# Performance work log

Hardware: AMD Instinct MI355X
Metric: run time of the kernel (lower is better)

Reference implementation:

```python
import jax, jax.numpy as jnp
import numpy as np

N, F, P, E, HID = 50000, 4, 12, 1_600_000, 64  # nodes, input feats, periods (FH), edges, hidden


def setup_inputs() -> dict:
    key = jax.random.key(0)
    ks = jax.random.split(key, 16)

    def nrm(k, shp, scale=0.1):
        return jax.random.normal(k, shp, jnp.float32) * scale

    inp = {
        "x": jax.random.normal(ks[0], (N, F, P), jnp.float32),
        "edge_index": jax.random.randint(ks[1], (2, E), 0, N),
        "edge_weights": jax.random.uniform(ks[2], (E,), jnp.float32),
        "att": nrm(ks[3], (P,), 1.0),
    }
    i = 4
    for g in ("z", "r", "h"):  # TGCN gate params: GCNConv weight/bias + Linear(2*hid, hid)
        inp[f"Wg_{g}"] = nrm(ks[i], (F, HID))
        inp[f"bg_{g}"] = jnp.zeros((HID,), jnp.float32)
        inp[f"Wl_{g}"] = nrm(jax.random.fold_in(ks[i], 1), (2 * HID, HID))
        inp[f"bl_{g}"] = jnp.zeros((HID,), jnp.float32)
        i += 1
    for j in range(1, 5):
        inp[f"W{j}"] = nrm(ks[i], (HID, HID))
        inp[f"b{j}"] = jnp.zeros((HID,), jnp.float32)
        i += 1
    inp["Wo"] = nrm(ks[i], (HID, P * F))
    inp["bo"] = jnp.zeros((P * F,), jnp.float32)
    return inp


def _gcn_norm(edge_index, ew):
    # GCNConv default: add self loops (weight 1), symmetric D^-1/2 (A+I) D^-1/2 normalization
    src, dst = edge_index[0], edge_index[1]
    loop = jnp.arange(N)
    src_f = jnp.concatenate([src, loop])
    dst_f = jnp.concatenate([dst, loop])
    ew_f = jnp.concatenate([ew, jnp.ones((N,), ew.dtype)])
    deg = jax.ops.segment_sum(ew_f, dst_f, num_segments=N)
    dinv = jnp.where(deg > 0, jax.lax.rsqrt(deg), 0.0)
    norm = dinv[src_f] * ew_f * dinv[dst_f]
    return src_f, dst_f, norm


def _gcn(x, W, b, src, dst, norm):
    xw = x @ W                               # [N, HID] transform before propagate
    msg = xw[src] * norm[:, None]            # gather + scale, [E+N, HID]
    return jax.ops.segment_sum(msg, dst, num_segments=N) + b


def reference(x, edge_index, edge_weights, att,
              Wg_z, bg_z, Wl_z, bl_z,
              Wg_r, bg_r, Wl_r, bl_r,
              Wg_h, bg_h, Wl_h, bl_h,
              W1, b1, W2, b2, W3, b3, W4, b4, Wo, bo):
    src, dst, norm = _gcn_norm(edge_index, edge_weights)

    def tgcn_cell(xt):
        # A3TGCN passes H=None every period -> H starts at zeros each period
        Hz = jnp.zeros((xt.shape[0], HID), xt.dtype)
        z = jax.nn.sigmoid(jnp.concatenate([_gcn(xt, Wg_z, bg_z, src, dst, norm), Hz], -1) @ Wl_z + bl_z)
        r = jax.nn.sigmoid(jnp.concatenate([_gcn(xt, Wg_r, bg_r, src, dst, norm), Hz], -1) @ Wl_r + bl_r)
        htil = jnp.tanh(jnp.concatenate([_gcn(xt, Wg_h, bg_h, src, dst, norm), Hz * r], -1) @ Wl_h + bl_h)
        return z * Hz + (1.0 - z) * htil

    probs = jax.nn.softmax(att)
    h = jnp.zeros((N, HID), x.dtype)
    for p in range(P):  # small fixed period loop keeps peak memory at one period's messages
        h = h + probs[p] * tgcn_cell(x[:, :, p])

    h = jax.nn.relu(h)
    h = h @ W1 + b1
    h = h @ W2 + b2
    h = h @ W3 + b3
    h = h @ W4 + b4
    h = h @ Wo + bo                          # [N, FH*F]
    return h.reshape(-1, F, P)
```

## Files before the change

kernel.cpp:

```cpp
#include <hip/hip_runtime.h>
#include <hip/hip_fp16.h>

#define FP 48
#define HID 64
#define NP 12
#define PL 65
#define NBB 256
#define BT 1024
#define CAPB 17920

__device__ __forceinline__ void mm_stage(const float* __restrict__ Alds,
                                         const float* __restrict__ Wg,
                                         float* __restrict__ Clds, int t)
{
    const int rg = (t >> 4) * 4, cg = (t & 15) * 4;
    float acc[4][4] = {};
    for (int k = 0; k < 64; ++k) {
        float a0 = Alds[(rg + 0) * PL + k];
        float a1 = Alds[(rg + 1) * PL + k];
        float a2 = Alds[(rg + 2) * PL + k];
        float a3 = Alds[(rg + 3) * PL + k];
        const float4 bv = *reinterpret_cast<const float4*>(Wg + k * 64 + cg);
        acc[0][0] += a0 * bv.x; acc[0][1] += a0 * bv.y; acc[0][2] += a0 * bv.z; acc[0][3] += a0 * bv.w;
        acc[1][0] += a1 * bv.x; acc[1][1] += a1 * bv.y; acc[1][2] += a1 * bv.z; acc[1][3] += a1 * bv.w;
        acc[2][0] += a2 * bv.x; acc[2][1] += a2 * bv.y; acc[2][2] += a2 * bv.z; acc[2][3] += a2 * bv.w;
        acc[3][0] += a3 * bv.x; acc[3][1] += a3 * bv.y; acc[3][2] += a3 * bv.z; acc[3][3] += a3 * bv.w;
    }
    for (int i = 0; i < 4; ++i)
        for (int j = 0; j < 4; ++j)
            Clds[(rg + i) * PL + cg + j] = acc[i][j];
}

__device__ __forceinline__ void bias_stage(const float* __restrict__ bin,
                                           const float* __restrict__ Wg,
                                           const float* __restrict__ badd,
                                           float* __restrict__ bout, int t)
{
    if (t < 64) {
        float s = badd[t];
        for (int k = 0; k < 64; ++k) s += bin[k] * Wg[k * 64 + t];
        bout[t] = s;
    }
}

__device__ void do_prep(
    const float* __restrict__ att,
    const float* __restrict__ Wg_z, const float* __restrict__ bg_z,
    const float* __restrict__ Wl_z, const float* __restrict__ bl_z,
    const float* __restrict__ Wg_h, const float* __restrict__ bg_h,
    const float* __restrict__ Wl_h, const float* __restrict__ bl_h,
    const float* __restrict__ W1, const float* __restrict__ b1,
    const float* __restrict__ W2, const float* __restrict__ b2,
    const float* __restrict__ W3, const float* __restrict__ b3,
    const float* __restrict__ W4, const float* __restrict__ b4,
    const float* __restrict__ Wo, const float* __restrict__ bo,
    float* __restrict__ probs, float* __restrict__ Mz, float* __restrict__ cz,
    float* __restrict__ Mh, float* __restrict__ ch,
    float* __restrict__ Wc, float* __restrict__ bc, int t)
{
    __shared__ float A[64 * PL];
    __shared__ float B[64 * PL];
    __shared__ float bias[64];
    __shared__ float bias2[64];

    if (t == 0) {
        float m = att[0];
        for (int p = 1; p < NP; ++p) m = fmaxf(m, att[p]);
        float e[NP]; float s = 0.f;
        for (int p = 0; p < NP; ++p) { e[p] = __expf(att[p] - m); s += e[p]; }
        float inv = 1.f / s;
        for (int p = 0; p < NP; ++p) probs[p] = e[p] * inv;
    }

    if (t < 256) {
        int f = t >> 6, j = t & 63;
        float az = 0.f, ah = 0.f;
        for (int k = 0; k < HID; ++k) {
            az += Wg_z[f * HID + k] * Wl_z[k * HID + j];
            ah += Wg_h[f * HID + k] * Wl_h[k * HID + j];
        }
        Mz[t] = az; Mh[t] = ah;
    }
    if (t < HID) {
        float az = bl_z[t], ah = bl_h[t];
        for (int k = 0; k < HID; ++k) {
            az += bg_z[k] * Wl_z[k * HID + t];
            ah += bg_h[k] * Wl_h[k * HID + t];
        }
        cz[t] = az; ch[t] = ah;
    }

    for (int idx = t; idx < 4096; idx += BT) {
        int i = idx >> 6, j = idx & 63;
        A[i * PL + j] = W1[idx];
    }
    if (t < 64) bias[t] = b1[t];
    __syncthreads();

    if (t < 256) mm_stage(A, W2, B, t);
    bias_stage(bias, W2, b2, bias2, t);
    __syncthreads();
    if (t < 256) mm_stage(B, W3, A, t);
    bias_stage(bias2, W3, b3, bias, t);
    __syncthreads();
    if (t < 256) mm_stage(A, W4, B, t);
    bias_stage(bias, W4, b4, bias2, t);
    __syncthreads();

    if (t < 256) {
        const int rg = (t >> 4) * 4, cg = (t & 15) * 4;
        if (cg < FP) {
            float acc[4][4] = {};
            for (int k = 0; k < 64; ++k) {
                float a0 = B[(rg + 0) * PL + k];
                float a1 = B[(rg + 1) * PL + k];
                float a2 = B[(rg + 2) * PL + k];
                float a3 = B[(rg + 3) * PL + k];
                const float4 bv = *reinterpret_cast<const float4*>(Wo + k * FP + cg);
                acc[0][0] += a0 * bv.x; acc[0][1] += a0 * bv.y; acc[0][2] += a0 * bv.z; acc[0][3] += a0 * bv.w;
                acc[1][0] += a1 * bv.x; acc[1][1] += a1 * bv.y; acc[1][2] += a1 * bv.z; acc[1][3] += a1 * bv.w;
                acc[2][0] += a2 * bv.x; acc[2][1] += a2 * bv.y; acc[2][2] += a2 * bv.z; acc[2][3] += a2 * bv.w;
                acc[3][0] += a3 * bv.x; acc[3][1] += a3 * bv.y; acc[3][2] += a3 * bv.z; acc[3][3] += a3 * bv.w;
            }
            for (int i = 0; i < 4; ++i)
                for (int j = 0; j < 4; ++j)
                    Wc[(rg + i) * FP + cg + j] = acc[i][j];
        }
        if (t < FP) {
            float s = bo[t];
            for (int k = 0; k < 64; ++k) s += bias2[k] * Wo[k * FP + t];
            bc[t] = s;
        }
    }
}

__global__ __launch_bounds__(BT) void build_kernel(
    const int* __restrict__ src, const int* __restrict__ dst,
    const float* __restrict__ ew,
    unsigned* __restrict__ cursor, int2* __restrict__ binned,
    int E, int CE, int NBUK,
    const float* __restrict__ att,
    const float* __restrict__ Wg_z, const float* __restrict__ bg_z,
    const float* __restrict__ Wl_z, const float* __restrict__ bl_z,
    const float* __restrict__ Wg_h, const float* __restrict__ bg_h,
    const float* __restrict__ Wl_h, const float* __restrict__ bl_h,
    const float* __restrict__ W1, const float* __restrict__ b1,
    const float* __restrict__ W2, const float* __restrict__ b2,
    const float* __restrict__ W3, const float* __restrict__ b3,
    const float* __restrict__ W4, const float* __restrict__ b4,
    const float* __restrict__ Wo, const float* __restrict__ bo,
    float* __restrict__ probs, float* __restrict__ Mz, float* __restrict__ cz,
    float* __restrict__ Mh, float* __restrict__ ch,
    float* __restrict__ Wc, float* __restrict__ bc)
{
    const int t = threadIdx.x;
    if (blockIdx.x == NBB) {
        do_prep(att, Wg_z, bg_z, Wl_z, bl_z, Wg_h, bg_h, Wl_h, bl_h,
                W1, b1, W2, b2, W3, b3, W4, b4, Wo, bo,
                probs, Mz, cz, Mh, ch, Wc, bc, t);
        return;
    }
    __shared__ int cnt[128];
    __shared__ int off[128];
    const int base = blockIdx.x * CE;
    const int endb = min(base + CE, E);
    if (t < NBUK) cnt[t] = 0;
    __syncthreads();
    for (int e = base + t; e < endb; e += BT)
        atomicAdd(&cnt[((unsigned)dst[e]) >> 9], 1);
    __syncthreads();
    if (t < NBUK) {
        const int c = cnt[t];
        off[t] = c ? (int)atomicAdd(&cursor[t], (unsigned)c) : 0;
    }
    __syncthreads();
    for (int e = base + t; e < endb; e += BT) {
        const int d = dst[e];
        const int b = ((unsigned)d) >> 9;
        const int r = atomicAdd(&off[b], 1);
        if (r < CAPB)
            binned[(size_t)b * CAPB + r] =
                make_int2(((d & 511) << 16) | src[e], __float_as_int(ew[e]));
    }
}

__global__ __launch_bounds__(1024) void csr_convert_kernel(
    const int2* __restrict__ binned, const unsigned* __restrict__ cursor,
    unsigned* __restrict__ csr, int2* __restrict__ nodeinfo,
    const float* __restrict__ x,
    unsigned short* __restrict__ xs, int N, int NBUK)
{
    const int t = threadIdx.x;
    const int b = blockIdx.x;
    const int node0 = b << 9;
    const int nend = min(512, N - node0);
    const int ebeg = b * CAPB;
    const int ecnt = min((int)cursor[b], CAPB);
    const int eend = ebeg + ecnt;

    __shared__ int   cnt[512];
    __shared__ float fsum[512];
    __shared__ int   pfx[512];
    __shared__ float sdi[512];

    if (t < 512) { cnt[t] = 0; fsum[t] = 0.f; }
    __syncthreads();

    for (int e = ebeg + t; e < eend; e += 1024) {
        const int2 v = binned[e];
        const int dl = (v.x >> 16) & 511;
        atomicAdd(&cnt[dl], 1);
        atomicAdd(&fsum[dl], __int_as_float(v.y));
    }
    __syncthreads();

    const int myc = (t < 512) ? cnt[t] : 0;
    if (t < 512) pfx[t] = myc;
    __syncthreads();
    for (int off = 1; off < 512; off <<= 1) {
        int tmp = (t >= off && t < 512) ? pfx[t - off] : 0;
        __syncthreads();
        if (t < 512) pfx[t] += tmp;
        __syncthreads();
    }

    if (t < 512) {
        const int excl = pfx[t] - myc;
        const float di = rsqrtf(1.f + fsum[t]);
        sdi[t] = di;
        if (t < nend)
            nodeinfo[node0 + t] = make_int2((myc << 22) | (ebeg + excl), __float_as_int(di));
        cnt[t] = ebeg + excl;
    }
    __syncthreads();

    for (int e = ebeg + t; e < eend; e += 1024) {
        const int2 v = binned[e];
        const int dl = (v.x >> 16) & 511;
        const int pos = atomicAdd(&cnt[dl], 1);
        const float w = __int_as_float(v.y);
        const unsigned hb = (unsigned)__half_as_ushort(__float2half_rn(w));
        csr[pos] = (unsigned)(v.x & 0xffff) | (hb << 16);
    }

    const int gtot = nend * 6;
    for (int g = t; g < gtot; g += 1024) {
        const int nl = g / 6;
        const int q = g - nl * 6;
        const float dsc = sdi[nl];
        const float* xr = x + (size_t)(node0 + nl) * FP + q * 8;
        const float4 v0 = *reinterpret_cast<const float4*>(xr);
        const float4 v1 = *reinterpret_cast<const float4*>(xr + 4);
        unsigned p0 = (unsigned)__half_as_ushort(__float2half_rn(dsc * v0.x)) |
                      ((unsigned)__half_as_ushort(__float2half_rn(dsc * v0.y)) << 16);
        unsigned p1 = (unsigned)__half_as_ushort(__float2half_rn(dsc * v0.z)) |
                      ((unsigned)__half_as_ushort(__float2half_rn(dsc * v0.w)) << 16);
        unsigned p2 = (unsigned)__half_as_ushort(__float2half_rn(dsc * v1.x)) |
                      ((unsigned)__half_as_ushort(__float2half_rn(dsc * v1.y)) << 16);
        unsigned p3 = (unsigned)__half_as_ushort(__float2half_rn(dsc * v1.z)) |
                      ((unsigned)__half_as_ushort(__float2half_rn(dsc * v1.w)) << 16);
        *reinterpret_cast<int4*>(xs + (size_t)(node0 + nl) * FP + q * 8) =
            make_int4((int)p0, (int)p1, (int)p2, (int)p3);
    }
}

__global__ __launch_bounds__(256) void gather_node_kernel(
    const unsigned short* __restrict__ xs, const float* __restrict__ x,
    const int2* __restrict__ nodeinfo,
    const unsigned* __restrict__ csr,
    const float* __restrict__ probs,
    const float* __restrict__ Mz, const float* __restrict__ cz,
    const float* __restrict__ Mh, const float* __restrict__ ch,
    const float* __restrict__ Wc, const float* __restrict__ bc,
    float* __restrict__ out, int N)
{
    __shared__ __align__(16) float sWc[HID * FP];
    __shared__ __align__(16) float sprobs[16];
    __shared__ __align__(16) float yacc[4][384];
    __shared__ __align__(16) float yld[4][FP];
    __shared__ __align__(16) float hld[4][HID];
    for (int i = threadIdx.x; i < HID * FP; i += 256) sWc[i] = Wc[i];
    if (threadIdx.x < NP) sprobs[threadIdx.x] = probs[threadIdx.x];
    __syncthreads();

    const int lane = threadIdx.x & 63;
    const int wib  = threadIdx.x >> 6;
    const int n    = blockIdx.x * 4 + wib;
    if (n >= N) return;

    const int slot = lane >> 3;
    const int q    = lane & 7;
    const bool act = (q < 6);
    const int qc   = act ? q : 5;
    const char* xsb = (const char*)xs;

    const int2 ni = nodeinfo[n];
    const int beg = ni.x & 0x3FFFFF;
    const int end = beg + (int)((unsigned)ni.x >> 22);
    const float di = __int_as_float(ni.y);

    float a0 = 0.f, a1 = 0.f, a2 = 0.f, a3 = 0.f;
    float a4 = 0.f, a5 = 0.f, a6 = 0.f, a7 = 0.f;
    #pragma unroll 2
    for (int e = beg + slot; e < end; e += 8) {
        const unsigned ev = csr[e];
        const float w = __half2float(__ushort_as_half((unsigned short)(ev >> 16)));
        const unsigned soff = (ev & 0xffffu) * 96u;
        const int4 xv = *reinterpret_cast<const int4*>(xsb + soff + (qc << 4));
        const float2 f0 = __half22float2(*reinterpret_cast<const __half2*>(&xv.x));
        const float2 f1 = __half22float2(*reinterpret_cast<const __half2*>(&xv.y));
        const float2 f2 = __half22float2(*reinterpret_cast<const __half2*>(&xv.z));
        const float2 f3 = __half22float2(*reinterpret_cast<const __half2*>(&xv.w));
        a0 = fmaf(w, f0.x, a0); a1 = fmaf(w, f0.y, a1);
        a2 = fmaf(w, f1.x, a2); a3 = fmaf(w, f1.y, a3);
        a4 = fmaf(w, f2.x, a4); a5 = fmaf(w, f2.y, a5);
        a6 = fmaf(w, f3.x, a6); a7 = fmaf(w, f3.y, a7);
    }

    if (act) {
        float* dst0 = &yacc[wib][slot * 48 + q * 8];
        *reinterpret_cast<float4*>(dst0)     = make_float4(a0, a1, a2, a3);
        *reinterpret_cast<float4*>(dst0 + 4) = make_float4(a4, a5, a6, a7);
    }

    if (lane < FP) {
        const float* yf = yacc[wib];
        float s = 0.f;
        #pragma unroll
        for (int sl = 0; sl < 8; ++sl) s += yf[sl * 48 + lane];
        float xself = x[(size_t)n * FP + lane];
        float yv = di * s + di * di * xself;
        int f = lane / 12;
        int p = lane - f * 12;
        yld[wib][p * 4 + f] = yv;
    }

    const float mz0 = Mz[lane], mz1 = Mz[64 + lane], mz2 = Mz[128 + lane], mz3 = Mz[192 + lane];
    const float mh0 = Mh[lane], mh1 = Mh[64 + lane], mh2 = Mh[128 + lane], mh3 = Mh[192 + lane];
    const float czv = cz[lane], chv = ch[lane];
    const int   c   = (lane < FP) ? lane : 0;
    const float bcv = bc[c];

    const float* yw = yld[wib];
    float hacc = 0.f;
    #pragma unroll
    for (int p = 0; p < NP; ++p) {
        const float4 v = *reinterpret_cast<const float4*>(yw + p * 4);
        float az = czv + v.x * mz0 + v.y * mz1 + v.z * mz2 + v.w * mz3;
        float ah = chv + v.x * mh0 + v.y * mh1 + v.z * mh2 + v.w * mh3;
        float g  = __builtin_amdgcn_rcpf(1.f + __expf(az));
        float ahc = fminf(fmaxf(ah, -15.f), 15.f);
        float eh = __expf(2.f * ahc);
        float th = 1.f - 2.f * __builtin_amdgcn_rcpf(eh + 1.f);
        hacc += sprobs[p] * g * th;
    }
    hacc = fmaxf(hacc, 0.f);

    hld[wib][lane] = hacc;
    const float* hw = hld[wib];
    float o = bcv;
    #pragma unroll
    for (int i4 = 0; i4 < 16; ++i4) {
        const float4 h4 = *reinterpret_cast<const float4*>(hw + i4 * 4);
        o += h4.x * sWc[(i4 * 4 + 0) * FP + c];
        o += h4.y * sWc[(i4 * 4 + 1) * FP + c];
        o += h4.z * sWc[(i4 * 4 + 2) * FP + c];
        o += h4.w * sWc[(i4 * 4 + 3) * FP + c];
    }
    if (lane < FP) out[(size_t)n * FP + lane] = o;
}

extern "C" void kernel_launch(void* const* d_in, const int* in_sizes, int n_in,
                              void* d_out, int out_size, void* d_ws, size_t ws_size,
                              hipStream_t stream)
{
    const int N = in_sizes[0] / FP;
    const int E = in_sizes[1] / 2;
    const int NBUK = (N + 511) >> 9;
    const int CE = (E + NBB - 1) / NBB;

    const float* x    = (const float*)d_in[0];
    const int*   ei   = (const int*)d_in[1];
    const float* ew   = (const float*)d_in[2];
    const float* att  = (const float*)d_in[3];
    const float* Wg_z = (const float*)d_in[4];
    const float* bg_z = (const float*)d_in[5];
    const float* Wl_z = (const float*)d_in[6];
    const float* bl_z = (const float*)d_in[7];
    const float* Wg_h = (const float*)d_in[12];
    const float* bg_h = (const float*)d_in[13];
    const float* Wl_h = (const float*)d_in[14];
    const float* bl_h = (const float*)d_in[15];
    const float* W1 = (const float*)d_in[16]; const float* b1 = (const float*)d_in[17];
    const float* W2 = (const float*)d_in[18]; const float* b2 = (const float*)d_in[19];
    const float* W3 = (const float*)d_in[20]; const float* b3 = (const float*)d_in[21];
    const float* W4 = (const float*)d_in[22]; const float* b4 = (const float*)d_in[23];
    const float* Wo = (const float*)d_in[24]; const float* bo = (const float*)d_in[25];

    const int* srcp = ei;
    const int* dstp = ei + E;

    int2* binned       = (int2*)d_ws;
    unsigned* csr      = (unsigned*)(binned + (size_t)NBUK * CAPB);
    unsigned short* xs = (unsigned short*)(csr + (size_t)NBUK * CAPB);
    unsigned* cursor   = (unsigned*)(xs + (size_t)N * FP);
    int2* nodeinfo     = (int2*)(cursor + 128);
    float* probs       = (float*)(nodeinfo + N);
    float* Mz          = probs + 16;
    float* cz          = Mz + 256;
    float* Mh          = cz + 64;
    float* ch          = Mh + 256;
    float* Wc          = ch + 64;
    float* bc          = Wc + HID * FP;

    hipMemsetAsync(cursor, 0, (size_t)NBUK * sizeof(unsigned), stream);

    build_kernel<<<NBB + 1, BT, 0, stream>>>(
        srcp, dstp, ew, cursor, binned, E, CE, NBUK,
        att, Wg_z, bg_z, Wl_z, bl_z, Wg_h, bg_h, Wl_h, bl_h,
        W1, b1, W2, b2, W3, b3, W4, b4, Wo, bo,
        probs, Mz, cz, Mh, ch, Wc, bc);

    csr_convert_kernel<<<NBUK, 1024, 0, stream>>>(binned, cursor, csr, nodeinfo,
                                                  x, xs, N, NBUK);

    gather_node_kernel<<<(N + 3) / 4, 256, 0, stream>>>(xs, x, nodeinfo, csr,
                                                        probs, Mz, cz, Mh, ch, Wc, bc,
                                                        (float*)d_out, N);
}
```

Measured before the change: 273.3 us.

## Use finer 128-node buckets, more build blocks, register-cached CSR conversion

Shrinks the destination buckets from 512 to 128 nodes, giving about 391 buckets. This spreads the CSR conversion over many more, smaller 512-thread blocks instead of 98 blocks of 1024 threads. The build kernel now uses 512 edge blocks and staggers its cursor atomics by block index to reduce contention. The conversion kernel loads each bucket's edges into registers once and reuses them for counting and scattering, rather than reading global memory twice. The cost is a fixed per-bucket capacity of 4864, only 10 edges per thread, and silent edge drops if a bucket overflows.

```diff
diff --git a/kernel.cpp b/kernel.cpp
--- a/kernel.cpp
+++ b/kernel.cpp
@@ -5,9 +5,10 @@
 #define HID 64
 #define NP 12
 #define PL 65
-#define NBB 256
+#define NBB 512
 #define BT 1024
-#define CAPB 17920
+#define CAPB 4864
+#define NBKMAX 512
 
 __device__ __forceinline__ void mm_stage(const float* __restrict__ Alds,
                                          const float* __restrict__ Wg,
@@ -160,31 +161,32 @@
                 probs, Mz, cz, Mh, ch, Wc, bc, t);
         return;
     }
-    __shared__ int cnt[128];
-    __shared__ int off[128];
+    __shared__ int cnt[NBKMAX];
+    __shared__ int off[NBKMAX];
     const int base = blockIdx.x * CE;
     const int endb = min(base + CE, E);
-    if (t < NBUK) cnt[t] = 0;
+    for (int i = t; i < NBUK; i += BT) cnt[i] = 0;
     __syncthreads();
     for (int e = base + t; e < endb; e += BT)
-        atomicAdd(&cnt[((unsigned)dst[e]) >> 9], 1);
-    __syncthreads();
-    if (t < NBUK) {
-        const int c = cnt[t];
-        off[t] = c ? (int)atomicAdd(&cursor[t], (unsigned)c) : 0;
+        atomicAdd(&cnt[((unsigned)dst[e]) >> 7], 1);
+    __syncthreads();
+    for (int i = t; i < NBUK; i += BT) {
+        const int idx = (i + (int)blockIdx.x) % NBUK;
+        const int c = cnt[idx];
+        off[idx] = c ? (int)atomicAdd(&cursor[idx], (unsigned)c) : 0;
     }
     __syncthreads();
     for (int e = base + t; e < endb; e += BT) {
         const int d = dst[e];
-        const int b = ((unsigned)d) >> 9;
-        const int r = atomicAdd(&off[b], 1);
+        const int bk = ((unsigned)d) >> 7;
+        const int r = atomicAdd(&off[bk], 1);
         if (r < CAPB)
-            binned[(size_t)b * CAPB + r] =
-                make_int2(((d & 511) << 16) | src[e], __float_as_int(ew[e]));
-    }
-}
-
-__global__ __launch_bounds__(1024) void csr_convert_kernel(
+            binned[(size_t)bk * CAPB + r] =
+                make_int2(((d & 127) << 16) | src[e], __float_as_int(ew[e]));
+    }
+}
+
+__global__ __launch_bounds__(512) void csr_convert_kernel(
     const int2* __restrict__ binned, const unsigned* __restrict__ cursor,
     unsigned* __restrict__ csr, int2* __restrict__ nodeinfo,
     const float* __restrict__ x,
@@ -192,39 +194,47 @@
 {
     const int t = threadIdx.x;
     const int b = blockIdx.x;
-    const int node0 = b << 9;
-    const int nend = min(512, N - node0);
+    const int node0 = b << 7;
+    const int nend = min(128, N - node0);
     const int ebeg = b * CAPB;
     const int ecnt = min((int)cursor[b], CAPB);
-    const int eend = ebeg + ecnt;
-
-    __shared__ int   cnt[512];
-    __shared__ float fsum[512];
-    __shared__ int   pfx[512];
-    __shared__ float sdi[512];
-
-    if (t < 512) { cnt[t] = 0; fsum[t] = 0.f; }
-    __syncthreads();
-
-    for (int e = ebeg + t; e < eend; e += 1024) {
-        const int2 v = binned[e];
-        const int dl = (v.x >> 16) & 511;
-        atomicAdd(&cnt[dl], 1);
-        atomicAdd(&fsum[dl], __int_as_float(v.y));
-    }
-    __syncthreads();
-
-    const int myc = (t < 512) ? cnt[t] : 0;
-    if (t < 512) pfx[t] = myc;
-    __syncthreads();
-    for (int off = 1; off < 512; off <<= 1) {
-        int tmp = (t >= off && t < 512) ? pfx[t - off] : 0;
+
+    __shared__ int   cnt[128];
+    __shared__ float fsum[128];
+    __shared__ int   pfx[128];
+    __shared__ float sdi[128];
+
+    if (t < 128) { cnt[t] = 0; fsum[t] = 0.f; }
+    __syncthreads();
+
+    int2 ev[10];
+    #pragma unroll
+    for (int i = 0; i < 10; ++i) {
+        const int o = i * 512 + t;
+        ev[i] = (o < ecnt) ? binned[ebeg + o] : make_int2(-1, 0);
+    }
+    #pragma unroll
+    for (int i = 0; i < 10; ++i) {
+        if (ev[i].x >= 0) {
+            const int dl = (ev[i].x >> 16) & 127;
+            atomicAdd(&cnt[dl], 1);
+            atomicAdd(&fsum[dl], __int_as_float(ev[i].y));
+        }
+    }
+    __syncthreads();
+
+    const int myc = (t < 128) ? cnt[t] : 0;
+    if (t < 128) pfx[t] = myc;
+    __syncthreads();
+    for (int off = 1; off < 128; off <<= 1) {
+        int tmp = 0;
+        if (t < 128 && t >= off) tmp = pfx[t - off];
         __syncthreads();
-        if (t < 512) pfx[t] += tmp;
+        if (t < 128 && t >= off) pfx[t] += tmp;
         __syncthreads();
     }
 
-    if (t < 512) {
+    if (t < 128) {
         const int excl = pfx[t] - myc;
         const float di = rsqrtf(1.f + fsum[t]);
         sdi[t] = di;
@@ -234,17 +244,19 @@
     }
     __syncthreads();
 
-    for (int e = ebeg + t; e < eend; e += 1024) {
-        const int2 v = binned[e];
-        const int dl = (v.x >> 16) & 511;
-        const int pos = atomicAdd(&cnt[dl], 1);
-        const float w = __int_as_float(v.y);
-        const unsigned hb = (unsigned)__half_as_ushort(__float2half_rn(w));
-        csr[pos] = (unsigned)(v.x & 0xffff) | (hb << 16);
+    #pragma unroll
+    for (int i = 0; i < 10; ++i) {
+        if (ev[i].x >= 0) {
+            const int dl = (ev[i].x >> 16) & 127;
+            const int pos = atomicAdd(&cnt[dl], 1);
+            const float w = __int_as_float(ev[i].y);
+            const unsigned hb = (unsigned)__half_as_ushort(__float2half_rn(w));
+            csr[pos] = (unsigned)(ev[i].x & 0xffff) | (hb << 16);
+        }
     }
 
     const int gtot = nend * 6;
-    for (int g = t; g < gtot; g += 1024) {
+    for (int g = t; g < gtot; g += 512) {
         const int nl = g / 6;
         const int q = g - nl * 6;
         const float dsc = sdi[nl];
@@ -376,7 +388,7 @@
 {
     const int N = in_sizes[0] / FP;
     const int E = in_sizes[1] / 2;
-    const int NBUK = (N + 511) >> 9;
+    const int NBUK = (N + 127) >> 7;
     const int CE = (E + NBB - 1) / NBB;
 
     const float* x    = (const float*)d_in[0];
@@ -404,7 +416,7 @@
     unsigned* csr      = (unsigned*)(binned + (size_t)NBUK * CAPB);
     unsigned short* xs = (unsigned short*)(csr + (size_t)NBUK * CAPB);
     unsigned* cursor   = (unsigned*)(xs + (size_t)N * FP);
-    int2* nodeinfo     = (int2*)(cursor + 128);
+    int2* nodeinfo     = (int2*)(cursor + 512);
     float* probs       = (float*)(nodeinfo + N);
     float* Mz          = probs + 16;
     float* cz          = Mz + 256;
@@ -421,8 +433,8 @@
         W1, b1, W2, b2, W3, b3, W4, b4, Wo, bo,
         probs, Mz, cz, Mh, ch, Wc, bc);
 
-    csr_convert_kernel<<<NBUK, 1024, 0, stream>>>(binned, cursor, csr, nodeinfo,
-                                                  x, xs, N, NBUK);
+    csr_convert_kernel<<<NBUK, 512, 0, stream>>>(binned, cursor, csr, nodeinfo,
+                                                 x, xs, N, NBUK);
 
     gather_node_kernel<<<(N + 3) / 4, 256, 0, stream>>>(xs, x, nodeinfo, csr,
                                                         probs, Mz, cz, Mh, ch, Wc, bc,
```

After: 264.1 us. 1.04x faster.
